# Kernel tuning notes

Hardware: AMD Instinct MI355X
Metric: run time of the kernel (lower is better)

Reference implementation:

```python
import jax, jax.numpy as jnp
import numpy as np

B, S, N, DIN, DOUT = 8, 2048, 16, 1024, 1024

def setup_inputs() -> dict:
    key = jax.random.key(0)
    k1, k2, k3, k4 = jax.random.split(key, 4)
    x = jax.random.normal(k1, (B, S, DIN), dtype=jnp.float32)
    # selection_probs: per-batch mixture weights over total_options (rows sum to 1)
    logits = jax.random.uniform(k2, (B, N), dtype=jnp.float32)
    selection_probs = jax.nn.softmax(logits, axis=-1)
    # kaiming_uniform(a=sqrt(5)) over fan_in=DIN -> bound = 1/sqrt(DIN)
    bound = 1.0 / np.sqrt(DIN)
    weight = jax.random.uniform(k3, (N, DOUT, DIN), dtype=jnp.float32, minval=-bound, maxval=bound)
    bias = jax.random.uniform(k4, (N, DOUT), dtype=jnp.float32, minval=-bound, maxval=bound)
    return {"x": x, "selection_probs": selection_probs, "weight": weight, "bias": bias}

def reference(x, selection_probs, weight, bias):
    # Math identical to: einsum('nij,baj->bani', W, x) then einsum('bani,bn->bai', ., p)
    # but mixes weights per-batch first (same contraction, avoids the [B,S,N,DOUT] tensor).
    mixed_w = jnp.einsum('bn,nij->bij', selection_probs, weight)   # [B, DOUT, DIN]
    out = jnp.einsum('bij,baj->bai', mixed_w, x)                   # [B, S, DOUT]
    mixed_b = jnp.einsum('bn,ni->bi', selection_probs, bias)       # [B, DOUT]
    return out + mixed_b[:, None, :]
```

## Files before the change

kernel.cpp:

```cpp
#include <hip/hip_runtime.h>
#include <hip/hip_bf16.h>
#include <stdint.h>

#define BB 8
#define SS 2048
#define NEXP 16
#define DIN 1024
#define DOUT 1024

typedef short bf16x8 __attribute__((ext_vector_type(8)));
typedef float floatx4 __attribute__((ext_vector_type(4)));

__device__ __forceinline__ unsigned short f2bf(float f) {
    union { float f; unsigned int u; } v; v.f = f;
    unsigned int u = v.u;
    unsigned int r = u + 0x7FFFu + ((u >> 16) & 1u);
    return (unsigned short)(r >> 16);
}

__device__ __forceinline__ void gload16(const void* g, void* l) {
    __builtin_amdgcn_global_load_lds(
        (const __attribute__((address_space(1))) void*)g,
        (__attribute__((address_space(3))) void*)l,
        16, 0, 0);
}

__global__ __launch_bounds__(256) void xconv_kernel(
    const float* __restrict__ x, const float* __restrict__ p,
    const float* __restrict__ bias,
    unsigned short* __restrict__ xb, float* __restrict__ mb)
{
    const long gid = (long)blockIdx.x * 256 + threadIdx.x;
    const long NX = (long)BB * SS * DIN / 8;
    if (gid < NX) {
        const float4* xv = (const float4*)x;
        float4 v0 = xv[gid * 2 + 0];
        float4 v1 = xv[gid * 2 + 1];
        uint4 o;
        o.x = (unsigned)f2bf(v0.x) | ((unsigned)f2bf(v0.y) << 16);
        o.y = (unsigned)f2bf(v0.z) | ((unsigned)f2bf(v0.w) << 16);
        o.z = (unsigned)f2bf(v1.x) | ((unsigned)f2bf(v1.y) << 16);
        o.w = (unsigned)f2bf(v1.z) | ((unsigned)f2bf(v1.w) << 16);
        ((uint4*)xb)[gid] = o;
    } else {
        const long t = gid - NX;
        if (t < (long)BB * DOUT) {
            const int b = (int)(t >> 10), i = (int)(t & 1023);
            float s = 0.f;
            #pragma unroll
            for (int n = 0; n < NEXP; ++n) s += p[b * NEXP + n] * bias[n * DOUT + i];
            mb[t] = s;
        }
    }
}

__global__ __launch_bounds__(256) void wmix_kernel(
    const float* __restrict__ p, const float* __restrict__ w,
    unsigned short* __restrict__ mw)
{
    __shared__ float sp[BB * NEXP];
    const int tid = threadIdx.x;
    if (tid < BB * NEXP) sp[tid] = p[tid];
    __syncthreads();

    const long t  = (long)blockIdx.x * 256 + tid;
    const long j4 = t * 4;
    float acc[BB][4];
    #pragma unroll
    for (int b = 0; b < BB; ++b)
        #pragma unroll
        for (int k = 0; k < 4; ++k) acc[b][k] = 0.f;
    #pragma unroll
    for (int n = 0; n < NEXP; ++n) {
        float4 wv = *(const float4*)(w + (long)n * DOUT * DIN + j4);
        #pragma unroll
        for (int b = 0; b < BB; ++b) {
            float pb = sp[b * NEXP + n];
            acc[b][0] += pb * wv.x; acc[b][1] += pb * wv.y;
            acc[b][2] += pb * wv.z; acc[b][3] += pb * wv.w;
        }
    }
    #pragma unroll
    for (int b = 0; b < BB; ++b) {
        uint2 o;
        o.x = (unsigned)f2bf(acc[b][0]) | ((unsigned)f2bf(acc[b][1]) << 16);
        o.y = (unsigned)f2bf(acc[b][2]) | ((unsigned)f2bf(acc[b][3]) << 16);
        *(uint2*)(mw + (long)b * DOUT * DIN + j4) = o;
    }
}

__global__ __launch_bounds__(256) void gemm_kernel(
    const unsigned short* __restrict__ xb,
    const unsigned short* __restrict__ mw,
    const float* __restrict__ mb,
    float* __restrict__ out)
{
    __shared__ __align__(16) unsigned short sA[128 * 64];
    __shared__ __align__(16) unsigned short sB[128 * 64];

    const int tid  = threadIdx.x;
    const int wave = tid >> 6;
    const int lane = tid & 63;
    const int b    = blockIdx.x;
    const int tileN = blockIdx.y * 128;
    const int tileM = blockIdx.z * 128;

    const unsigned short* Ag = xb + (long)b * SS * DIN;
    const unsigned short* Bg = mw + (long)b * DOUT * DIN;

    const int q     = lane >> 4;
    const int r16   = lane & 15;
    const int mBase = 64 * (wave >> 1);
    const int nBase = 64 * (wave & 1);

    const int sRow = (lane >> 3);
    const int sColSw = (((lane & 7) ^ sRow) * 8);

    const int swz = (r16 & 7);

    floatx4 acc[4][4];
    #pragma unroll
    for (int mi = 0; mi < 4; ++mi)
        #pragma unroll
        for (int ni = 0; ni < 4; ++ni)
            acc[mi][ni] = (floatx4){0.f, 0.f, 0.f, 0.f};

    for (int k0 = 0; k0 < DIN; k0 += 64) {
        __syncthreads();
        #pragma unroll
        for (int c = 0; c < 4; ++c) {
            const int chunk = wave * 4 + c;
            const int row   = chunk * 8 + sRow;
            gload16(Ag + (long)(tileM + row) * DIN + k0 + sColSw, &sA[chunk * 512]);
            gload16(Bg + (long)(tileN + row) * DIN + k0 + sColSw, &sB[chunk * 512]);
        }
        __syncthreads();

        #pragma unroll
        for (int kk = 0; kk < 64; kk += 32) {
            const int gA = ((kk >> 3) + q);
            bf16x8 af[4], bfv[4];
            #pragma unroll
            for (int i = 0; i < 4; ++i)
                af[i] = *(const bf16x8*)&sA[(mBase + 16 * i + r16) * 64 + ((gA ^ swz) * 8)];
            #pragma unroll
            for (int i = 0; i < 4; ++i)
                bfv[i] = *(const bf16x8*)&sB[(nBase + 16 * i + r16) * 64 + ((gA ^ swz) * 8)];
            #pragma unroll
            for (int mi = 0; mi < 4; ++mi)
                #pragma unroll
                for (int ni = 0; ni < 4; ++ni)
                    acc[mi][ni] = __builtin_amdgcn_mfma_f32_16x16x32_bf16(
                        af[mi], bfv[ni], acc[mi][ni], 0, 0, 0);
        }
    }

    float bv[4];
    #pragma unroll
    for (int ni = 0; ni < 4; ++ni)
        bv[ni] = mb[b * DOUT + tileN + nBase + 16 * ni + r16];

    #pragma unroll
    for (int mi = 0; mi < 4; ++mi) {
        #pragma unroll
        for (int rr = 0; rr < 4; ++rr) {
            const int row = tileM + mBase + 16 * mi + q * 4 + rr;
            float* orow = out + (long)b * SS * DOUT + (long)row * DOUT;
            #pragma unroll
            for (int ni = 0; ni < 4; ++ni)
                orow[tileN + nBase + 16 * ni + r16] = acc[mi][ni][rr] + bv[ni];
        }
    }
}

extern "C" void kernel_launch(void* const* d_in, const int* in_sizes, int n_in,
                              void* d_out, int out_size, void* d_ws, size_t ws_size,
                              hipStream_t stream) {
    const float* x    = (const float*)d_in[0];
    const float* p    = (const float*)d_in[1];
    const float* w    = (const float*)d_in[2];
    const float* bias = (const float*)d_in[3];
    float* out = (float*)d_out;

    unsigned short* xb = (unsigned short*)d_ws;
    unsigned short* mw = (unsigned short*)((char*)d_ws + (size_t)33554432);
    float*          mb = (float*)((char*)d_ws + (size_t)33554432 + 16777216);

    xconv_kernel<<<dim3(8192 + 32), 256, 0, stream>>>(x, p, bias, xb, mb);
    wmix_kernel<<<dim3(1024), 256, 0, stream>>>(p, w, mw);

    dim3 ggrid(BB, DOUT / 128, SS / 128);
    gemm_kernel<<<ggrid, 256, 0, stream>>>(xb, mw, mb, out);
}
```

Baseline: 214.7 us.

## Give each wave private LDS tiles and drop block-level barriers in GEMM

Each of the four waves now stages its own 64x64 A and B sub-tiles into a private LDS slice. The two per-iteration __syncthreads are replaced by wave-local waitcnt instructions, so waves no longer stall on each other and can drift out of phase. The cost is that every wave loads its own data: global/L2 load traffic per block doubles, and LDS use per block doubles to 64KB, which can lower the number of resident blocks per CU. There is still no double buffering, so each wave still waits for its loads to finish before computing.

```diff
diff --git a/kernel.cpp b/kernel.cpp
--- a/kernel.cpp
+++ b/kernel.cpp
@@ -10,6 +10,9 @@
 
 typedef short bf16x8 __attribute__((ext_vector_type(8)));
 typedef float floatx4 __attribute__((ext_vector_type(4)));
+
+#define WAIT_VM0()   __builtin_amdgcn_s_waitcnt(0x0f70)
+#define WAIT_LGKM0() __builtin_amdgcn_s_waitcnt(0xc07f)
 
 __device__ __forceinline__ unsigned short f2bf(float f) {
     union { float f; unsigned int u; } v; v.f = f;
@@ -95,8 +98,8 @@
     const float* __restrict__ mb,
     float* __restrict__ out)
 {
-    __shared__ __align__(16) unsigned short sA[128 * 64];
-    __shared__ __align__(16) unsigned short sB[128 * 64];
+    __shared__ __align__(16) unsigned short sA[4][64 * 64];
+    __shared__ __align__(16) unsigned short sB[4][64 * 64];
 
     const int tid  = threadIdx.x;
     const int wave = tid >> 6;
@@ -110,11 +113,14 @@
 
     const int q     = lane >> 4;
     const int r16   = lane & 15;
-    const int mBase = 64 * (wave >> 1);
-    const int nBase = 64 * (wave & 1);
+    const int mBase = tileM + 64 * (wave >> 1);
+    const int nBase = tileN + 64 * (wave & 1);
 
-    const int sRow = (lane >> 3);
+    const int sRow   = lane >> 3;
     const int sColSw = (((lane & 7) ^ sRow) * 8);
+
+    unsigned short* myA = &sA[wave][0];
+    unsigned short* myB = &sB[wave][0];
 
     const int swz = (r16 & 7);
 
@@ -126,15 +132,14 @@
             acc[mi][ni] = (floatx4){0.f, 0.f, 0.f, 0.f};
 
     for (int k0 = 0; k0 < DIN; k0 += 64) {
-        __syncthreads();
+        WAIT_LGKM0();
         #pragma unroll
-        for (int c = 0; c < 4; ++c) {
-            const int chunk = wave * 4 + c;
-            const int row   = chunk * 8 + sRow;
-            gload16(Ag + (long)(tileM + row) * DIN + k0 + sColSw, &sA[chunk * 512]);
-            gload16(Bg + (long)(tileN + row) * DIN + k0 + sColSw, &sB[chunk * 512]);
+        for (int c = 0; c < 8; ++c) {
+            const int row = c * 8 + sRow;
+            gload16(Ag + (long)(mBase + row) * DIN + k0 + sColSw, myA + c * 512);
+            gload16(Bg + (long)(nBase + row) * DIN + k0 + sColSw, myB + c * 512);
         }
-        __syncthreads();
+        WAIT_VM0();
 
         #pragma unroll
         for (int kk = 0; kk < 64; kk += 32) {
@@ -142,10 +147,10 @@
             bf16x8 af[4], bfv[4];
             #pragma unroll
             for (int i = 0; i < 4; ++i)
-                af[i] = *(const bf16x8*)&sA[(mBase + 16 * i + r16) * 64 + ((gA ^ swz) * 8)];
+                af[i] = *(const bf16x8*)&myA[(16 * i + r16) * 64 + ((gA ^ swz) * 8)];
             #pragma unroll
             for (int i = 0; i < 4; ++i)
-                bfv[i] = *(const bf16x8*)&sB[(nBase + 16 * i + r16) * 64 + ((gA ^ swz) * 8)];
+                bfv[i] = *(const bf16x8*)&myB[(16 * i + r16) * 64 + ((gA ^ swz) * 8)];
             #pragma unroll
             for (int mi = 0; mi < 4; ++mi)
                 #pragma unroll
@@ -158,17 +163,17 @@
     float bv[4];
     #pragma unroll
     for (int ni = 0; ni < 4; ++ni)
-        bv[ni] = mb[b * DOUT + tileN + nBase + 16 * ni + r16];
+        bv[ni] = mb[b * DOUT + nBase + 16 * ni + r16];
 
     #pragma unroll
     for (int mi = 0; mi < 4; ++mi) {
         #pragma unroll
         for (int rr = 0; rr < 4; ++rr) {
-            const int row = tileM + mBase + 16 * mi + q * 4 + rr;
+            const int row = mBase + 16 * mi + q * 4 + rr;
             float* orow = out + (long)b * SS * DOUT + (long)row * DOUT;
             #pragma unroll
             for (int ni = 0; ni < 4; ++ni)
-                orow[tileN + nBase + 16 * ni + r16] = acc[mi][ni][rr] + bv[ni];
+                orow[nBase + 16 * ni + r16] = acc[mi][ni][rr] + bv[ni];
         }
     }
 }
```

Result: slower. 219.3 us (+2.2%).
